# Kernel optimization log

Hardware: AMD Instinct MI355X
Metric: run time of the kernel (lower is better)

Reference implementation:

```python
import jax, jax.numpy as jnp
import numpy as np

NEG = -1000000.0  # mask fill value used by the torch module


def setup_inputs() -> dict:
    key = jax.random.key(0)
    kq, kk, kv, km = jax.random.split(key, 4)
    B, Q, K, D = 8, 2048, 2048, 128
    queries = jax.random.normal(kq, (B, Q, D), dtype=jnp.float32)
    keys = jax.random.normal(kk, (B, K, D), dtype=jnp.float32)
    values = jax.random.normal(kv, (B, K, D), dtype=jnp.float32)
    attntion_mask = jax.random.randint(km, (B, K), 0, 2, dtype=jnp.int32)
    return {"queries": queries, "keys": keys, "values": values,
            "attntion_mask": attntion_mask}


def reference(queries, keys, values, attntion_mask):
    d = queries.shape[-1]
    # scores: [B, Q, K]
    scores = jnp.einsum('bqd,bkd->bqk', queries, keys) / jnp.sqrt(
        jnp.asarray(d, dtype=queries.dtype))
    # 2D mask [B, K] broadcasts over the query axis (torch repeat_interleave)
    mask = attntion_mask.astype(bool)[:, None, :]  # [B, 1, K]
    scores = jnp.where(mask, scores, NEG)
    weights = jax.nn.softmax(scores, axis=-1)
    # dropout rate is 0.0 (eval mode) -> identity
    return jnp.einsum('bqk,bkv->bqv', weights, values)
```

## Files before the change

### kernel.cpp

```cpp
#include <hip/hip_runtime.h>
#include <stdint.h>

typedef __attribute__((ext_vector_type(8))) short short8;
typedef __attribute__((ext_vector_type(4))) float f32x4;

#define NB 8
#define NQ 2048
#define NK 2048
#define ND 128
#define SCALE 0.08838834764831845f
#define L2E   1.4426950408889634f
#define FMAXC 10.0f

__device__ __forceinline__ uint32_t pk_bf16(float a, float b) {
  uint32_t ua = __builtin_bit_cast(uint32_t, a);
  uint32_t ub = __builtin_bit_cast(uint32_t, b);
  ua += 0x7FFFu + ((ua >> 16) & 1u);
  ub += 0x7FFFu + ((ub >> 16) & 1u);
  return (ua >> 16) | (ub & 0xFFFF0000u);
}

__device__ __forceinline__ void dma16(const void* g, void* l) {
  __builtin_amdgcn_global_load_lds((const __attribute__((address_space(1))) void*)g,
                                   (__attribute__((address_space(3))) void*)l, 16, 0, 0);
}

__global__ __launch_bounds__(256) void compact_kernel(const int* __restrict__ maskm,
                                                      int* __restrict__ idxArr,
                                                      int* __restrict__ KcArr) {
  __shared__ int cnt;
  const int b = blockIdx.x;
  const int t = threadIdx.x;
  const int lane = t & 63;
  if (t == 0) cnt = 0;
  __syncthreads();
#pragma unroll
  for (int j = 0; j < 8; ++j) {
    int k = t * 8 + j;
    bool bit = maskm[b * NK + k] != 0;
    unsigned long long m = __ballot(bit);
    int pre = __popcll(m & ((1ull << lane) - 1ull));
    int tot = __popcll(m);
    int base = 0;
    if (lane == 0 && tot) base = atomicAdd(&cnt, tot);
    base = __shfl(base, 0);
    if (bit) idxArr[b * NK + base + pre] = k;
  }
  __syncthreads();
  int kc = cnt;
  for (int s = kc + t; s < NK; s += 256) idxArr[b * NK + s] = -1;
  if (t == 0) KcArr[b] = kc;
}

__global__ __launch_bounds__(256) void prep_kernel(const float* __restrict__ v,
                                                   const float* __restrict__ kin,
                                                   ushort* __restrict__ vt,
                                                   ushort* __restrict__ kb,
                                                   const int* __restrict__ idxArr) {
  const int t = threadIdx.x;
  const int bid = blockIdx.x;
  if (bid < 512) {
    __shared__ __align__(16) float tile[4096];
    char* sm = (char*)tile;
    const int b = bid >> 6;
    const int k0 = ((bid >> 1) & 31) << 6;
    const int d0 = (bid & 1) << 6;
#pragma unroll
    for (int i = 0; i < 4; ++i) {
      int id = i * 256 + t;
      int k = id >> 4, c = id & 15;
      int src = idxArr[b * NK + k0 + k];
      uint4 val; val.x = 0u; val.y = 0u; val.z = 0u; val.w = 0u;
      if (src >= 0) val = *(const uint4*)(v + (size_t)(b * NK + src) * ND + d0 + c * 4);
      *(uint4*)(sm + k * 256 + ((c ^ (k & 15)) * 16)) = val;
    }
    __syncthreads();
#pragma unroll
    for (int i = 0; i < 2; ++i) {
      int id = i * 256 + t;
      int d = id >> 3, kc = id & 7;
      uint32_t w[4];
#pragma unroll
      for (int jj = 0; jj < 4; ++jj) {
        int kA = kc * 8 + jj * 2, kB = kA + 1;
        float fa = *(const float*)(sm + kA * 256 + (((d >> 2) ^ (kA & 15)) * 16) + (d & 3) * 4);
        float fb = *(const float*)(sm + kB * 256 + (((d >> 2) ^ (kB & 15)) * 16) + (d & 3) * 4);
        w[jj] = pk_bf16(fa, fb);
      }
      uint4 o; o.x = w[0]; o.y = w[1]; o.z = w[2]; o.w = w[3];
      *(uint4*)(vt + (size_t)(b * ND + d0 + d) * NK + k0 + kc * 8) = o;
    }
  } else {
    const int kblk = bid - 512;
#pragma unroll
    for (int pass = 0; pass < 8; ++pass) {
      int gs = kblk * 128 + pass * 16 + (t >> 4);
      int src = idxArr[gs];
      int col = (t & 15) * 8;
      uint4 u; u.x = 0u; u.y = 0u; u.z = 0u; u.w = 0u;
      if (src >= 0) {
        int b2 = gs >> 11;
        const float* p = kin + (size_t)(b2 * NK + src) * ND + col;
        f32x4 a = *(const f32x4*)p;
        f32x4 c = *(const f32x4*)(p + 4);
        u.x = pk_bf16(a[0], a[1]); u.y = pk_bf16(a[2], a[3]);
        u.z = pk_bf16(c[0], c[1]); u.w = pk_bf16(c[2], c[3]);
      }
      *(uint4*)(kb + (size_t)gs * ND + col) = u;
    }
  }
}

template <bool MASKED>
__device__ __forceinline__ void do_softmax(const f32x4 st[2], float& l_,
                                           char* pbase, int r, int quad, int rem) {
  const float C1 = SCALE * L2E;
  const float C2 = -FMAXC * L2E;
  float p[2][4]; float ps = 0.f;
#pragma unroll
  for (int mt = 0; mt < 2; ++mt) {
    float t0 = fmaf(st[mt][0], C1, C2);
    float t1 = fmaf(st[mt][1], C1, C2);
    float t2 = fmaf(st[mt][2], C1, C2);
    float t3 = fmaf(st[mt][3], C1, C2);
    if (MASKED) {
      const int rm = rem - mt * 16;
      t0 = (rm > 0) ? t0 : -2.0e6f;
      t1 = (rm > 1) ? t1 : -2.0e6f;
      t2 = (rm > 2) ? t2 : -2.0e6f;
      t3 = (rm > 3) ? t3 : -2.0e6f;
    }
    p[mt][0] = exp2f(t0); p[mt][1] = exp2f(t1);
    p[mt][2] = exp2f(t2); p[mt][3] = exp2f(t3);
    ps += p[mt][0] + p[mt][1] + p[mt][2] + p[mt][3];
  }
  l_ += ps;
#pragma unroll
  for (int mt = 0; mt < 2; ++mt) {
    uint2 w; w.x = pk_bf16(p[mt][0], p[mt][1]); w.y = pk_bf16(p[mt][2], p[mt][3]);
    *(uint2*)(pbase + r * 64 + (((mt * 4 + quad) ^ (r & 6)) * 8)) = w;
  }
}

#define LDS_BYTES 106496
__global__ __launch_bounds__(512) void attn_kernel(const float* __restrict__ qm,
                                                   const ushort* __restrict__ kbm,
                                                   const ushort* __restrict__ vtm,
                                                   const int* __restrict__ KcArr,
                                                   float* __restrict__ outm) {
  __shared__ __align__(16) char sm[LDS_BYTES];
  const int o   = blockIdx.x;
  const int bid = (o & 7) * 32 + (o >> 3);
  const int b   = bid >> 5;
  const int q0  = (bid & 31) << 6;
  const int t = threadIdx.x;
  const int lane = t & 63;
  const int wave = t >> 6;
  const int r = lane & 15;
  const int quad = lane >> 4;
  const int qg = wave >> 1;
  const int kq = wave & 1;

  const int Kc   = KcArr[b];
  const int n_it = (Kc + 63) >> 6;
  const int CH   = n_it << 5;

  uint32_t koff[2], voff[2];
#pragma unroll
  for (int j = 0; j < 2; ++j) {
    int i = wave * 2 + j;
    int rho = i * 4 + (lane >> 4);
    int ck = (lane & 15) ^ (rho & 15);
    koff[j] = (uint32_t)(b * NK + (rho >> 5) * CH + (rho & 31)) * ND + ck * 8;
    int u = i * 16 + (lane >> 2);
    int cv = (lane & 3) ^ (u & 3);
    voff[j] = (uint32_t)(b * ND + (u & 127)) * NK + (u >> 7) * CH + cv * 8;
  }

#define ISSUE_TILE(tt, bufi)                                                    \
  {                                                                             \
    const uint32_t kadd_ = (uint32_t)(tt) * 32 * ND;                            \
    const uint32_t vadd_ = (uint32_t)(tt) * 32;                                 \
    char* kb_ = sm + (bufi) * 16384;                                            \
    char* vb_ = sm + 49152 + (bufi) * 16384;                                    \
    _Pragma("unroll")                                                           \
    for (int j = 0; j < 2; ++j) {                                               \
      dma16(kbm + koff[j] + kadd_, kb_ + (wave * 2 + j) * 1024);                \
      dma16(vtm + voff[j] + vadd_, vb_ + (wave * 2 + j) * 1024);                \
    }                                                                           \
  }

  f32x4 qraw[4][2];
#pragma unroll
  for (int ks = 0; ks < 4; ++ks) {
    const float* p = qm + (size_t)(b * NQ + q0 + qg * 16 + r) * ND + ks * 32 + quad * 8;
    qraw[ks][0] = *(const f32x4*)p;
    qraw[ks][1] = *(const f32x4*)(p + 4);
  }
  ISSUE_TILE(0, 0);
  if (n_it > 1) ISSUE_TILE(1, 1);
  short8 qf[4];
#pragma unroll
  for (int ks = 0; ks < 4; ++ks) {
    uint4 u;
    u.x = pk_bf16(qraw[ks][0][0], qraw[ks][0][1]);
    u.y = pk_bf16(qraw[ks][0][2], qraw[ks][0][3]);
    u.z = pk_bf16(qraw[ks][1][0], qraw[ks][1][1]);
    u.w = pk_bf16(qraw[ks][1][2], qraw[ks][1][3]);
    qf[ks] = __builtin_bit_cast(short8, u);
  }

  f32x4 oacc[8];
#pragma unroll
  for (int dt = 0; dt < 8; ++dt) oacc[dt] = (f32x4){0.f, 0.f, 0.f, 0.f};
  float l_ = 0.f;

  char* const pbase = sm + 98304 + wave * 1024;

  const int vlim0 = Kc - kq * CH;

  int cur = 0;
  for (int it = 0; it < n_it; ++it) {
    if (it + 1 < n_it) asm volatile("s_waitcnt vmcnt(4)" ::: "memory");
    else               asm volatile("s_waitcnt vmcnt(0)" ::: "memory");
    __builtin_amdgcn_sched_barrier(0);
    __builtin_amdgcn_s_barrier();
    __builtin_amdgcn_sched_barrier(0);

    if (it + 2 < n_it) {
      int b2 = cur + 2; if (b2 >= 3) b2 -= 3;
      ISSUE_TILE(it + 2, b2);
    }

    char* const kcur = sm + cur * 16384 + kq * 8192;
    char* const vcur = sm + 49152 + cur * 16384 + kq * 8192;

    f32x4 st[2];
#pragma unroll
    for (int mt = 0; mt < 2; ++mt) {
      short8 kf[4];
#pragma unroll
      for (int ks = 0; ks < 4; ++ks)
        kf[ks] = *(const short8*)(kcur + (mt * 16 + r) * 256 + (((ks * 4 + quad) ^ r) * 16));
      f32x4 acc = (f32x4){0.f, 0.f, 0.f, 0.f};
#pragma unroll
      for (int ks = 0; ks < 4; ++ks)
        acc = __builtin_amdgcn_mfma_f32_16x16x32_bf16(kf[ks], qf[ks], acc, 0, 0, 0);
      st[mt] = acc;
    }

    const int vlim = vlim0 - it * 32;
    if (vlim >= 32) do_softmax<false>(st, l_, pbase, r, quad, 0);
    else            do_softmax<true >(st, l_, pbase, r, quad, vlim - quad * 4);
    short8 pf = *(const short8*)(pbase + r * 64 + (((quad * 2) ^ (r & 6)) * 8));

#pragma unroll
    for (int dt = 0; dt < 8; ++dt) {
      short8 vf = *(const short8*)(vcur + (dt * 16 + r) * 64 + ((quad ^ (r & 3)) * 16));
      oacc[dt] = __builtin_amdgcn_mfma_f32_16x16x32_bf16(vf, pf, oacc[dt], 0, 0, 0);
    }

    cur = (cur == 2) ? 0 : cur + 1;
  }

  __syncthreads();
  float* xch = (float*)(sm + qg * 9216) + lane * 36;
  if (kq == 1) {
    xch[0] = l_;
#pragma unroll
    for (int dt = 0; dt < 8; ++dt)
      *(f32x4*)(xch + 4 + dt * 4) = oacc[dt];
  }
  __syncthreads();
  if (kq == 0) {
    const int qrow = b * NQ + q0 + qg * 16 + r;
    float ls = l_ + xch[0];
    ls += __shfl_xor(ls, 16);
    ls += __shfl_xor(ls, 32);
    float inv = 1.0f / ls;
#pragma unroll
    for (int dt = 0; dt < 8; ++dt) {
      f32x4 o1 = *(const f32x4*)(xch + 4 + dt * 4);
      f32x4 ov = oacc[dt];
      ov[0] = (ov[0] + o1[0]) * inv;
      ov[1] = (ov[1] + o1[1]) * inv;
      ov[2] = (ov[2] + o1[2]) * inv;
      ov[3] = (ov[3] + o1[3]) * inv;
      *(f32x4*)(outm + (size_t)qrow * ND + dt * 16 + quad * 4) = ov;
    }
  }
#undef ISSUE_TILE
}

extern "C" void kernel_launch(void* const* d_in, const int* in_sizes, int n_in,
                              void* d_out, int out_size, void* d_ws, size_t ws_size,
                              hipStream_t stream) {
  const float* q   = (const float*)d_in[0];
  const float* k   = (const float*)d_in[1];
  const float* v   = (const float*)d_in[2];
  const int*   msk = (const int*)d_in[3];
  float* out = (float*)d_out;
  ushort* kb = (ushort*)d_ws;
  ushort* vt = kb + (size_t)NB * NK * ND;
  int* idxA  = (int*)(vt + (size_t)NB * NK * ND);
  int* kcA   = idxA + (size_t)NB * NK;

  compact_kernel<<<NB, 256, 0, stream>>>(msk, idxA, kcA);
  prep_kernel<<<640, 256, 0, stream>>>(v, k, vt, kb, idxA);
  attn_kernel<<<256, 512, 0, stream>>>(q, kb, vt, kcA, out);
}
```

Baseline: 107.2 us.

## Fuse mask compaction, K/V prep and attention into one cooperative kernel

Merges the three launches (mask compaction, K/V bf16 conversion and transpose, attention) into a single cooperative kernel. Each block recomputes the compacted index map for its batch in LDS, converts its own slice of K and V, and then waits on a grid-wide sync before running attention. This removes two kernel launches, the index array round-trip through global memory, and the inter-kernel gaps. In exchange it adds a grid sync and redundant per-block compaction, and with 256 blocks of 512 threads using large LDS it depends on every block being co-resident.

```diff
diff --git a/kernel.cpp b/kernel.cpp
--- a/kernel.cpp
+++ b/kernel.cpp
@@ -1,5 +1,8 @@
 #include <hip/hip_runtime.h>
+#include <hip/hip_cooperative_groups.h>
 #include <stdint.h>
+
+namespace cg = cooperative_groups;
 
 typedef __attribute__((ext_vector_type(8))) short short8;
 typedef __attribute__((ext_vector_type(4))) float f32x4;
@@ -23,92 +26,6 @@
 __device__ __forceinline__ void dma16(const void* g, void* l) {
   __builtin_amdgcn_global_load_lds((const __attribute__((address_space(1))) void*)g,
                                    (__attribute__((address_space(3))) void*)l, 16, 0, 0);
-}
-
-__global__ __launch_bounds__(256) void compact_kernel(const int* __restrict__ maskm,
-                                                      int* __restrict__ idxArr,
-                                                      int* __restrict__ KcArr) {
-  __shared__ int cnt;
-  const int b = blockIdx.x;
-  const int t = threadIdx.x;
-  const int lane = t & 63;
-  if (t == 0) cnt = 0;
-  __syncthreads();
-#pragma unroll
-  for (int j = 0; j < 8; ++j) {
-    int k = t * 8 + j;
-    bool bit = maskm[b * NK + k] != 0;
-    unsigned long long m = __ballot(bit);
-    int pre = __popcll(m & ((1ull << lane) - 1ull));
-    int tot = __popcll(m);
-    int base = 0;
-    if (lane == 0 && tot) base = atomicAdd(&cnt, tot);
-    base = __shfl(base, 0);
-    if (bit) idxArr[b * NK + base + pre] = k;
-  }
-  __syncthreads();
-  int kc = cnt;
-  for (int s = kc + t; s < NK; s += 256) idxArr[b * NK + s] = -1;
-  if (t == 0) KcArr[b] = kc;
-}
-
-__global__ __launch_bounds__(256) void prep_kernel(const float* __restrict__ v,
-                                                   const float* __restrict__ kin,
-                                                   ushort* __restrict__ vt,
-                                                   ushort* __restrict__ kb,
-                                                   const int* __restrict__ idxArr) {
-  const int t = threadIdx.x;
-  const int bid = blockIdx.x;
-  if (bid < 512) {
-    __shared__ __align__(16) float tile[4096];
-    char* sm = (char*)tile;
-    const int b = bid >> 6;
-    const int k0 = ((bid >> 1) & 31) << 6;
-    const int d0 = (bid & 1) << 6;
-#pragma unroll
-    for (int i = 0; i < 4; ++i) {
-      int id = i * 256 + t;
-      int k = id >> 4, c = id & 15;
-      int src = idxArr[b * NK + k0 + k];
-      uint4 val; val.x = 0u; val.y = 0u; val.z = 0u; val.w = 0u;
-      if (src >= 0) val = *(const uint4*)(v + (size_t)(b * NK + src) * ND + d0 + c * 4);
-      *(uint4*)(sm + k * 256 + ((c ^ (k & 15)) * 16)) = val;
-    }
-    __syncthreads();
-#pragma unroll
-    for (int i = 0; i < 2; ++i) {
-      int id = i * 256 + t;
-      int d = id >> 3, kc = id & 7;
-      uint32_t w[4];
-#pragma unroll
-      for (int jj = 0; jj < 4; ++jj) {
-        int kA = kc * 8 + jj * 2, kB = kA + 1;
-        float fa = *(const float*)(sm + kA * 256 + (((d >> 2) ^ (kA & 15)) * 16) + (d & 3) * 4);
-        float fb = *(const float*)(sm + kB * 256 + (((d >> 2) ^ (kB & 15)) * 16) + (d & 3) * 4);
-        w[jj] = pk_bf16(fa, fb);
-      }
-      uint4 o; o.x = w[0]; o.y = w[1]; o.z = w[2]; o.w = w[3];
-      *(uint4*)(vt + (size_t)(b * ND + d0 + d) * NK + k0 + kc * 8) = o;
-    }
-  } else {
-    const int kblk = bid - 512;
-#pragma unroll
-    for (int pass = 0; pass < 8; ++pass) {
-      int gs = kblk * 128 + pass * 16 + (t >> 4);
-      int src = idxArr[gs];
-      int col = (t & 15) * 8;
-      uint4 u; u.x = 0u; u.y = 0u; u.z = 0u; u.w = 0u;
-      if (src >= 0) {
-        int b2 = gs >> 11;
-        const float* p = kin + (size_t)(b2 * NK + src) * ND + col;
-        f32x4 a = *(const f32x4*)p;
-        f32x4 c = *(const f32x4*)(p + 4);
-        u.x = pk_bf16(a[0], a[1]); u.y = pk_bf16(a[2], a[3]);
-        u.z = pk_bf16(c[0], c[1]); u.w = pk_bf16(c[2], c[3]);
-      }
-      *(uint4*)(kb + (size_t)gs * ND + col) = u;
-    }
-  }
 }
 
 template <bool MASKED>
@@ -143,16 +60,19 @@
 }
 
 #define LDS_BYTES 106496
-__global__ __launch_bounds__(512) void attn_kernel(const float* __restrict__ qm,
-                                                   const ushort* __restrict__ kbm,
-                                                   const ushort* __restrict__ vtm,
-                                                   const int* __restrict__ KcArr,
-                                                   float* __restrict__ outm) {
+__global__ __launch_bounds__(512) void fused_kernel(const float* __restrict__ qm,
+                                                    const float* __restrict__ kin,
+                                                    const float* __restrict__ vin,
+                                                    const int* __restrict__ maskm,
+                                                    ushort* __restrict__ kbm,
+                                                    ushort* __restrict__ vtm,
+                                                    float* __restrict__ outm) {
   __shared__ __align__(16) char sm[LDS_BYTES];
   const int o   = blockIdx.x;
   const int bid = (o & 7) * 32 + (o >> 3);
   const int b   = bid >> 5;
-  const int q0  = (bid & 31) << 6;
+  const int qb  = bid & 31;
+  const int q0  = qb << 6;
   const int t = threadIdx.x;
   const int lane = t & 63;
   const int wave = t >> 6;
@@ -161,7 +81,101 @@
   const int qg = wave >> 1;
   const int kq = wave & 1;
 
-  const int Kc   = KcArr[b];
+  int* const slotmap = (int*)(sm + 98304);
+  int* const wsum    = (int*)(sm + 32768);
+
+  int4 mv = *(const int4*)(maskm + b * NK + t * 4);
+  int bits = (mv.x != 0) | ((mv.y != 0) << 1) | ((mv.z != 0) << 2) | ((mv.w != 0) << 3);
+  unsigned long long bl0 = __ballot(bits & 1);
+  unsigned long long bl1 = __ballot((bits >> 1) & 1);
+  unsigned long long bl2 = __ballot((bits >> 2) & 1);
+  unsigned long long bl3 = __ballot((bits >> 3) & 1);
+  unsigned long long below = (1ull << lane) - 1ull;
+  int tot0 = __popcll(bl0), tot1 = __popcll(bl1), tot2 = __popcll(bl2), tot3 = __popcll(bl3);
+  if (lane == 0) wsum[wave] = tot0 + tot1 + tot2 + tot3;
+  __syncthreads();
+  int wbase = 0, Kc = 0;
+#pragma unroll
+  for (int w = 0; w < 8; ++w) {
+    int s = wsum[w];
+    if (w < wave) wbase += s;
+    Kc += s;
+  }
+  int p0 = wbase + __popcll(bl0 & below);
+  int p1 = wbase + tot0 + __popcll(bl1 & below);
+  int p2 = wbase + tot0 + tot1 + __popcll(bl2 & below);
+  int p3 = wbase + tot0 + tot1 + tot2 + __popcll(bl3 & below);
+  if (mv.x) slotmap[p0] = t * 4 + 0;
+  if (mv.y) slotmap[p1] = t * 4 + 1;
+  if (mv.z) slotmap[p2] = t * 4 + 2;
+  if (mv.w) slotmap[p3] = t * 4 + 3;
+  for (int s = Kc + t; s < NK; s += 512) slotmap[s] = -1;
+  __syncthreads();
+
+  {
+    const int tile = t >> 8;
+    const int tt = t & 255;
+    const int vb = qb * 2 + tile;
+    const int k0 = (vb >> 1) << 6;
+    const int d0 = (vb & 1) << 6;
+    char* smt = sm + tile * 16384;
+#pragma unroll
+    for (int i = 0; i < 4; ++i) {
+      int id = i * 256 + tt;
+      int kk = id >> 4, c = id & 15;
+      int src = slotmap[k0 + kk];
+      uint4 val; val.x = 0u; val.y = 0u; val.z = 0u; val.w = 0u;
+      if (src >= 0) val = *(const uint4*)(vin + (size_t)(b * NK + src) * ND + d0 + c * 4);
+      *(uint4*)(smt + kk * 256 + ((c ^ (kk & 15)) * 16)) = val;
+    }
+    __syncthreads();
+#pragma unroll
+    for (int i = 0; i < 2; ++i) {
+      int id = i * 256 + tt;
+      int d = id >> 3, kc = id & 7;
+      uint32_t w[4];
+#pragma unroll
+      for (int jj = 0; jj < 4; ++jj) {
+        int kA = kc * 8 + jj * 2, kB = kA + 1;
+        float fa = *(const float*)(smt + kA * 256 + (((d >> 2) ^ (kA & 15)) * 16) + (d & 3) * 4);
+        float fb = *(const float*)(smt + kB * 256 + (((d >> 2) ^ (kB & 15)) * 16) + (d & 3) * 4);
+        w[jj] = pk_bf16(fa, fb);
+      }
+      uint4 ov; ov.x = w[0]; ov.y = w[1]; ov.z = w[2]; ov.w = w[3];
+      *(uint4*)(vtm + (size_t)(b * ND + d0 + d) * NK + k0 + kc * 8) = ov;
+    }
+  }
+
+#pragma unroll
+  for (int pass = 0; pass < 2; ++pass) {
+    int slot = qb * 64 + pass * 32 + (t >> 4);
+    int src = slotmap[slot];
+    int col = (t & 15) * 8;
+    uint4 u; u.x = 0u; u.y = 0u; u.z = 0u; u.w = 0u;
+    if (src >= 0) {
+      const float* p = kin + (size_t)(b * NK + src) * ND + col;
+      f32x4 a = *(const f32x4*)p;
+      f32x4 c = *(const f32x4*)(p + 4);
+      u.x = pk_bf16(a[0], a[1]); u.y = pk_bf16(a[2], a[3]);
+      u.z = pk_bf16(c[0], c[1]); u.w = pk_bf16(c[2], c[3]);
+    }
+    *(uint4*)(kbm + (size_t)(b * NK + slot) * ND + col) = u;
+  }
+
+  short8 qf[4];
+#pragma unroll
+  for (int ks = 0; ks < 4; ++ks) {
+    const float* p = qm + (size_t)(b * NQ + q0 + qg * 16 + r) * ND + ks * 32 + quad * 8;
+    f32x4 a = *(const f32x4*)p;
+    f32x4 c = *(const f32x4*)(p + 4);
+    uint4 u;
+    u.x = pk_bf16(a[0], a[1]); u.y = pk_bf16(a[2], a[3]);
+    u.z = pk_bf16(c[0], c[1]); u.w = pk_bf16(c[2], c[3]);
+    qf[ks] = __builtin_bit_cast(short8, u);
+  }
+
+  cg::this_grid().sync();
+
   const int n_it = (Kc + 63) >> 6;
   const int CH   = n_it << 5;
 
@@ -190,25 +204,8 @@
     }                                                                           \
   }
 
-  f32x4 qraw[4][2];
-#pragma unroll
-  for (int ks = 0; ks < 4; ++ks) {
-    const float* p = qm + (size_t)(b * NQ + q0 + qg * 16 + r) * ND + ks * 32 + quad * 8;
-    qraw[ks][0] = *(const f32x4*)p;
-    qraw[ks][1] = *(const f32x4*)(p + 4);
-  }
   ISSUE_TILE(0, 0);
   if (n_it > 1) ISSUE_TILE(1, 1);
-  short8 qf[4];
-#pragma unroll
-  for (int ks = 0; ks < 4; ++ks) {
-    uint4 u;
-    u.x = pk_bf16(qraw[ks][0][0], qraw[ks][0][1]);
-    u.y = pk_bf16(qraw[ks][0][2], qraw[ks][0][3]);
-    u.z = pk_bf16(qraw[ks][1][0], qraw[ks][1][1]);
-    u.w = pk_bf16(qraw[ks][1][2], qraw[ks][1][3]);
-    qf[ks] = __builtin_bit_cast(short8, u);
-  }
 
   f32x4 oacc[8];
 #pragma unroll
@@ -216,7 +213,6 @@
   float l_ = 0.f;
 
   char* const pbase = sm + 98304 + wave * 1024;
-
   const int vlim0 = Kc - kq * CH;
 
   int cur = 0;
@@ -302,10 +298,9 @@
   float* out = (float*)d_out;
   ushort* kb = (ushort*)d_ws;
   ushort* vt = kb + (size_t)NB * NK * ND;
-  int* idxA  = (int*)(vt + (size_t)NB * NK * ND);
-  int* kcA   = idxA + (size_t)NB * NK;
-
-  compact_kernel<<<NB, 256, 0, stream>>>(msk, idxA, kcA);
-  prep_kernel<<<640, 256, 0, stream>>>(v, k, vt, kb, idxA);
-  attn_kernel<<<256, 512, 0, stream>>>(q, kb, vt, kcA, out);
-}
+
+  void* args[] = {(void*)&q, (void*)&k, (void*)&v, (void*)&msk,
+                  (void*)&kb, (void*)&vt, (void*)&out};
+  hipLaunchCooperativeKernel((const void*)fused_kernel, dim3(256), dim3(512),
+                             args, 0, stream);
+}
```

After: 144.7 us. 1.35x slower.
